# Performance work log

Hardware: AMD Instinct MI355X
Metric: run time of the kernel (lower is better)

Reference implementation:

```python
import jax, jax.numpy as jnp
import numpy as np

DIM = 1024
NUM_HEADS = 8
HEAD_DIM = 64
QK_DIM = NUM_HEADS * HEAD_DIM  # 512
B, S = 4, 1024


def setup_inputs() -> dict:
    key = jax.random.key(0)
    k1, k2, k3, k4, k5 = jax.random.split(key, 5)
    x = jax.random.normal(k1, (B, S, DIM), dtype=jnp.float32)
    mask = jax.random.randint(k2, (B, S), 0, 2).astype(bool)
    rotator = jax.random.normal(k3, (B, S, HEAD_DIM, HEAD_DIM), dtype=jnp.float32)
    # Linear weights stored as [in, out] for x @ W
    w_t = jax.random.normal(k4, (DIM, 2 * QK_DIM + DIM), dtype=jnp.float32) * (DIM ** -0.5)
    w_o = jax.random.normal(k5, (DIM, DIM), dtype=jnp.float32) * (DIM ** -0.5)
    return {"x": x, "mask": mask, "rotator": rotator, "w_t": w_t, "w_o": w_o}


def taylor_atn_fn(qs, ks, vs, mask):
    # 2nd-order Taylor approximation of softmax attention:
    # exp(s) ~= 1 + s + s^2/2, with invalid keys masked out.
    scale = HEAD_DIM ** -0.5
    s = jnp.einsum('bqhd,bkhd->bhqk', qs, ks) * scale  # [B,H,S,S]
    scores = 1.0 + s + 0.5 * s * s
    scores = scores * mask[:, None, None, :].astype(scores.dtype)  # mask keys
    denom = jnp.maximum(jnp.sum(scores, axis=-1), 1e-6)            # [B,H,Q]
    out = jnp.einsum('bhqk,bkhd->bqhd', scores, vs)
    out = out / jnp.transpose(denom, (0, 2, 1))[..., None]         # [B,Q,H,vd]
    return out.reshape(out.shape[0], out.shape[1], -1)


def reference(x, mask, rotator, w_t, w_o):
    t = x @ w_t                                   # [B,S,2*QK+DIM]
    Bx, Sx = t.shape[0], t.shape[1]
    qs = t[..., :QK_DIM].reshape(Bx, Sx, NUM_HEADS, HEAD_DIM)
    ks = t[..., QK_DIM:2 * QK_DIM].reshape(Bx, Sx, NUM_HEADS, HEAD_DIM)
    vs = t[..., 2 * QK_DIM:].reshape(Bx, Sx, NUM_HEADS, -1)
    m = mask[..., None, None]
    # masked per-position rotation: q -> R q, k -> R^T k
    qs = jnp.where(m, jnp.einsum('bsij,bshj->bshi', rotator, qs), qs)
    ks = jnp.where(m, jnp.einsum('bsij,bshi->bshj', rotator, ks), ks)
    out = taylor_atn_fn(qs, ks, vs, mask)
    return out @ w_o
```

## Files before the change

kernel.cpp:

```cpp
#include <hip/hip_runtime.h>
#include <cstdint>
#include <cstddef>

#define DIMX  1024
#define NH    8
#define HD    64
#define QKD   512
#define VDD   128
#define BATCH 4
#define SEQ   1024
#define NPOS  (BATCH*SEQ)
#define TW    (2*QKD + DIMX)
#define SCALE 0.125f

typedef __bf16 bf16x8 __attribute__((ext_vector_type(8)));
typedef float  f32x4  __attribute__((ext_vector_type(4)));
typedef float  f32x16 __attribute__((ext_vector_type(16)));

__device__ __forceinline__ ushort f2bf(float f) {
    unsigned b = __float_as_uint(f);
    return (ushort)((b + 0x7FFFu + ((b >> 16) & 1u)) >> 16);
}
__device__ __forceinline__ float bf2f(ushort u) {
    return __uint_as_float((unsigned)u << 16);
}

__device__ __forceinline__ unsigned cvtpk(float lo, float hi) {
    unsigned r;
    asm("v_cvt_pk_bf16_f32 %0, %1, %2" : "=v"(r) : "v"(lo), "v"(hi));
    return r;
}

__device__ __forceinline__ void plswap(unsigned &a, unsigned &b) {
    asm("v_permlane32_swap_b32 %0, %1" : "+v"(a), "+v"(b));
}

#define GLD16(src, dst) __builtin_amdgcn_global_load_lds(                      \
    (const __attribute__((address_space(1))) unsigned int*)(src),              \
    (__attribute__((address_space(3))) unsigned int*)(dst), 16, 0, 0)

#define SW(row, col) ((row)*64 + ((col) ^ (((row)&7)<<3)))

__device__ __forceinline__ int2 xcd_swz(int gx, int gy) {
    const int nwg = gx * gy;
    int id = blockIdx.y * gx + blockIdx.x;
    id = (id & 7) * (nwg >> 3) + (id >> 3);
    return make_int2(id % gx, id / gx);
}

__global__ __launch_bounds__(256)
void prep_all(const float* __restrict__ x, const float* __restrict__ w_t,
              const float* __restrict__ w_o, ushort* __restrict__ xbf,
              ushort* __restrict__ wtT, ushort* __restrict__ woT)
{
    __shared__ float tile[32][33];
    const int bid = blockIdx.x;
    if (bid < 2048) {
        const size_t i = ((size_t)bid * 256 + threadIdx.x) * 8;
        float4 v0 = *(const float4*)(x + i);
        float4 v1 = *(const float4*)(x + i + 4);
        ushort o[8] = {f2bf(v0.x), f2bf(v0.y), f2bf(v0.z), f2bf(v0.w),
                       f2bf(v1.x), f2bf(v1.y), f2bf(v1.z), f2bf(v1.w)};
        *(uint4*)(xbf + i) = *(uint4*)o;
        return;
    }
    const float* W; ushort* WT; int K, N, bn, bk;
    if (bid < 4096) {
        W = w_t; WT = wtT; K = DIMX; N = TW;
        const int t = bid - 2048;
        bn = (t & 63) * 32; bk = (t >> 6) * 32;
    } else {
        W = w_o; WT = woT; K = DIMX; N = DIMX;
        const int t = bid - 4096;
        bn = (t & 31) * 32; bk = (t >> 5) * 32;
    }
    const int tx = threadIdx.x & 31;
    const int ty = threadIdx.x >> 5;
    #pragma unroll
    for (int i = ty; i < 32; i += 8)
        tile[i][tx] = W[(size_t)(bk + i) * N + bn + tx];
    __syncthreads();
    #pragma unroll
    for (int i = ty; i < 32; i += 8)
        WT[(size_t)(bn + i) * K + bk + tx] = f2bf(tile[tx][i]);
}

#define GEMM_PROLOGUE(Aptr, Bptr, Kdim)                                        \
    __shared__ __align__(16) ushort lA[2 * 128 * 64];                          \
    __shared__ __align__(16) ushort lB[2 * 128 * 64];                          \
    const int tid  = threadIdx.x;                                              \
    const int lane = tid & 63;                                                 \
    const int wave = tid >> 6;                                                 \
    const int wr   = wave >> 1;                                                \
    const int wc   = wave & 1;                                                 \
    const int rsub = lane >> 3;                        \
    const int scol = ((lane & 7) * 8) ^ ((rsub & 7) << 3);                     \
    const ushort* aP = (Aptr) + (size_t)(bm + wave*32 + rsub) * (Kdim) + scol; \
    const ushort* bP = (Bptr) + (size_t)(bn + wave*32 + rsub) * (Kdim) + scol; \
    ushort* lAw = lA + wave * 2048;                                            \
    ushort* lBw = lB + wave * 2048;                                            \
    const int fr = lane & 15;                                                  \
    const int l4 = lane >> 4;                                                  \
    f32x4 acc[4][4] = {};

#define GSTAGE(buf, k0, Kdim)                                                  \
    do {                                                                       \
        _Pragma("unroll")                                                      \
        for (int c = 0; c < 4; ++c) {                                          \
            GLD16(aP + (size_t)(c*8) * (Kdim) + (k0), lAw + (buf)*8192 + c*512);\
            GLD16(bP + (size_t)(c*8) * (Kdim) + (k0), lBw + (buf)*8192 + c*512);\
        }                                                                      \
    } while (0)

#define GEMM_KLOOP(Kdim)                                                       \
    GSTAGE(0, 0, Kdim);                                                        \
    for (int t = 0; t < (Kdim)/64; ++t) {                                      \
        const int cur = t & 1;                                                 \
        if (t < (Kdim)/64 - 1) {                                               \
            GSTAGE(cur ^ 1, (t + 1) * 64, Kdim);                               \
            asm volatile("s_waitcnt vmcnt(8)" ::: "memory");                   \
        } else {                                                               \
            asm volatile("s_waitcnt vmcnt(0)" ::: "memory");                   \
        }                                                                      \
        __builtin_amdgcn_s_barrier();               \
        _Pragma("unroll")                                                      \
        for (int ks = 0; ks < 2; ++ks) {                                       \
            bf16x8 af[4], bfr[4];                                              \
            _Pragma("unroll")                                                  \
            for (int m = 0; m < 4; ++m)                                        \
                af[m] = *(const bf16x8*)&lA[cur*8192 +                         \
                    SW(wr*64 + m*16 + fr, ks*32 + l4*8)];                      \
            _Pragma("unroll")                                                  \
            for (int n = 0; n < 4; ++n)                                        \
                bfr[n] = *(const bf16x8*)&lB[cur*8192 +                        \
                    SW(wc*64 + n*16 + fr, ks*32 + l4*8)];                      \
            _Pragma("unroll")                                                  \
            for (int m = 0; m < 4; ++m)                                        \
                _Pragma("unroll")                                              \
                for (int n = 0; n < 4; ++n)                                    \
                    acc[m][n] = __builtin_amdgcn_mfma_f32_16x16x32_bf16(       \
                        af[m], bfr[n], acc[m][n], 0, 0, 0);                    \
        }                                                                      \
        asm volatile("s_waitcnt lgkmcnt(0)" ::: "memory");                     \
        __builtin_amdgcn_s_barrier();             \
    }

__global__ __launch_bounds__(256, 2)
void gemm_qkv(const ushort* __restrict__ A, const ushort* __restrict__ BT,
              ushort* __restrict__ t1b, ushort* __restrict__ Vt)
{
    const int2 bij = xcd_swz(TW/128, NPOS/128);
    const int bm = bij.y * 128;
    const int bn = bij.x * 128;
    GEMM_PROLOGUE(A, BT, DIMX)
    GEMM_KLOOP(DIMX)

    const int orow = l4 * 4;
    if (bn < 1024) {
        #pragma unroll
        for (int m = 0; m < 4; ++m)
            #pragma unroll
            for (int n = 0; n < 4; ++n) {
                ushort* dst = t1b + (size_t)(bm + wr * 64 + m * 16 + orow) * 1024
                                  + bn + wc * 64 + n * 16 + fr;
                #pragma unroll
                for (int q = 0; q < 4; ++q)
                    dst[(size_t)q * 1024] = f2bf(acc[m][n][q]);
            }
    } else {
        #pragma unroll
        for (int m = 0; m < 4; ++m)
            #pragma unroll
            for (int n = 0; n < 4; ++n) {
                const int row0 = bm + wr * 64 + m * 16 + orow;
                const int cv   = bn + wc * 64 + n * 16 + fr - 1024;
                const int hh = cv >> 7, vd = cv & 127;
                const int bb = row0 >> 10, ss = row0 & 1023;
                ushort o4[4];
                #pragma unroll
                for (int q = 0; q < 4; ++q) o4[q] = f2bf(acc[m][n][q]);
                *(ushort4*)&Vt[((size_t)(bb*NH + hh)*VDD + vd)*SEQ + ss] =
                    *(ushort4*)o4;
            }
    }
}

__global__ __launch_bounds__(256, 2)
void gemm_bf16_mfma(const ushort* __restrict__ A, const ushort* __restrict__ BT,
                    float* __restrict__ C)
{
    const int2 bij = xcd_swz(DIMX/128, NPOS/128);
    const int bm = bij.y * 128;
    const int bn = bij.x * 128;
    GEMM_PROLOGUE(A, BT, DIMX)
    GEMM_KLOOP(DIMX)

    const int orow = l4 * 4;
    #pragma unroll
    for (int m = 0; m < 4; ++m)
        #pragma unroll
        for (int n = 0; n < 4; ++n) {
            float* dst = C + (size_t)(bm + wr * 64 + m * 16 + orow) * DIMX
                           + bn + wc * 64 + n * 16 + fr;
            #pragma unroll
            for (int q = 0; q < 4; ++q)
                dst[(size_t)q * DIMX] = acc[m][n][q];
        }
}

__global__ __launch_bounds__(256)
void rotate_pack_qk(const ushort* __restrict__ t1b, const int* __restrict__ mask,
                    const float* __restrict__ rot, ushort* __restrict__ Qb,
                    ushort* __restrict__ Kb)
{
    const int p   = blockIdx.x;
    const int tid = threadIdx.x;
    const int b = p >> 10, s = p & 1023;
    const bool rotated = (mask[p] != 0);

    __shared__ float R[64][69];
    __shared__ float qv[QKD];
    __shared__ float kv[QKD];

    const ushort* tq = t1b + (size_t)p * 1024;
    {
        ushort2 q2 = *(const ushort2*)(tq + tid*2);
        ushort2 k2 = *(const ushort2*)(tq + QKD + tid*2);
        qv[tid*2]   = bf2f(q2.x); qv[tid*2+1] = bf2f(q2.y);
        kv[tid*2]   = bf2f(k2.x); kv[tid*2+1] = bf2f(k2.y);
        if (rotated) {
            const float* Rg = rot + (size_t)p * 4096;
            const int base = tid * 16;
            const int r = base >> 6, c = base & 63;
            #pragma unroll
            for (int x = 0; x < 16; x += 4) {
                float4 v = *(const float4*)(Rg + base + x);
                R[r][c+x+0] = v.x; R[r][c+x+1] = v.y;
                R[r][c+x+2] = v.z; R[r][c+x+3] = v.w;
            }
        }
    }
    __syncthreads();

    #pragma unroll
    for (int ph = 0; ph < 2; ++ph) {
        const int h = (tid >> 6) + ph*4;
        const int i = tid & 63;
        const float* qh  = &qv[h*64];
        const float* kh2 = &kv[h*64];
        float aq, ak;
        if (rotated) {
            aq = 0.f; ak = 0.f;
            #pragma unroll 8
            for (int j = 0; j < 64; ++j) {
                aq = fmaf(R[i][j], qh[j], aq);
                ak = fmaf(R[j][i], kh2[j], ak);
            }
        } else {
            aq = qh[i]; ak = kh2[i];
        }
        const size_t dst = ((size_t)(b*NH + h)*SEQ + s)*HD + i;
        Qb[dst] = f2bf(aq * SCALE);
        Kb[dst] = f2bf(ak);
    }
}

__global__ __launch_bounds__(256, 2)
void taylor_attn_mfma(const ushort* __restrict__ Qb, const ushort* __restrict__ Kb,
                      const ushort* __restrict__ Vt, const int* __restrict__ mask,
                      ushort* __restrict__ attn)
{
    const int bh  = blockIdx.x;
    const int qt  = blockIdx.y;
    const int b   = bh >> 3, h = bh & 7;
    const int tid = threadIdx.x;
    const int lane = tid & 63;
    const int wave = tid >> 6;
    const int kh  = wave >> 1;
    const int qg  = wave & 1;
    const int l31 = lane & 31;
    const int g   = lane >> 5;

    __shared__ __align__(16) ushort smem[32768];
    __shared__ float mskAll[SEQ];
    __shared__ float dpart[64];
    __shared__ float dinv2[64];

    ushort* Ksp = smem + kh * 8192;
    ushort* Vsp = smem + 16384 + kh * 8192;
    float*  comb = (float*)smem;

    {
        int4 mv = *(const int4*)(mask + b*SEQ + tid*4);
        float4 f = make_float4(mv.x ? 1.f : 0.f, mv.y ? 1.f : 0.f,
                               mv.z ? 1.f : 0.f, mv.w ? 1.f : 0.f);
        *(float4*)&mskAll[tid*4] = f;
    }

    const ushort* qrow = Qb + ((size_t)bh*SEQ + qt*64 + qg*32 + l31) * HD + g*8;
    bf16x8 qf[4];
    #pragma unroll
    for (int ds = 0; ds < 4; ++ds) qf[ds] = *(const bf16x8*)(qrow + ds*16);

    const int sub  = lane >> 3;
    const int scol = ((lane & 7) * 8) ^ (sub << 3);
    const ushort* Kbase = Kb + (size_t)bh*SEQ*HD;
    const ushort* Vbase = Vt + (size_t)bh*VDD*SEQ;

#define ISSUE_K(buf, ktn) do {                                                 \
    _Pragma("unroll")                                                          \
    for (int i_ = 0; i_ < 4; ++i_)                                             \
        GLD16(Kbase + ((size_t)(ktn)*64 + 8*(qg*4+i_) + sub)*HD + scol,        \
              Ksp + (buf)*4096 + (qg*4+i_)*512);                               \
} while (0)
#define ISSUE_V(ktn) do {                                                      \
    _Pragma("unroll")                                                          \
    for (int i_ = 0; i_ < 8; ++i_)                                             \
        GLD16(Vbase + (size_t)(8*(qg*8+i_) + sub)*SEQ + (ktn)*64 + scol,       \
              Vsp + (qg*8+i_)*512);                                            \
} while (0)

    f32x16 acc[4] = {};
    float dacc = 0.f;

    __syncthreads();
    ISSUE_K(0, kh*8);

    for (int it = 0; it < 8; ++it) {
        const int kt = kh*8 + it;
        const int cb = it & 1;
        ISSUE_V(kt);
        if (it < 7) {
            ISSUE_K(cb ^ 1, kt + 1);
            asm volatile("s_waitcnt vmcnt(12)" ::: "memory");
        } else {
            asm volatile("s_waitcnt vmcnt(8)"  ::: "memory");
        }
        __builtin_amdgcn_s_barrier();

        f32x16 sf0 = {}, sf1 = {};
        __builtin_amdgcn_s_setprio(1);
        #pragma unroll
        for (int ds = 0; ds < 4; ++ds) {
            const int dc = ds*16 + g*8;
            bf16x8 kf0 = *(const bf16x8*)&Ksp[cb*4096 + SW(l31, dc)];
            bf16x8 kf1 = *(const bf16x8*)&Ksp[cb*4096 + SW(32 + l31, dc)];
            sf0 = __builtin_amdgcn_mfma_f32_32x32x16_bf16(kf0, qf[ds], sf0, 0, 0, 0);
            sf1 = __builtin_amdgcn_mfma_f32_32x32x16_bf16(kf1, qf[ds], sf1, 0, 0, 0);
        }
        __builtin_amdgcn_s_setprio(0);

        const float* mrow = mskAll + kt*64;
        unsigned w0[8], w1[8];
        float dadd = 0.f;
        #pragma unroll
        for (int rr = 0; rr < 4; ++rr) {
            const float4 mqa = *(const float4*)&mrow[8*rr + 4*g];
            const float4 mqb = *(const float4*)&mrow[32 + 8*rr + 4*g];
            float s0 = sf0[rr*4+0], s1 = sf0[rr*4+1];
            float s2 = sf0[rr*4+2], s3 = sf0[rr*4+3];
            float c0 = fmaf(fmaf(0.5f*s0, s0, s0), mqa.x, mqa.x);
            float c1 = fmaf(fmaf(0.5f*s1, s1, s1), mqa.y, mqa.y);
            float c2 = fmaf(fmaf(0.5f*s2, s2, s2), mqa.z, mqa.z);
            float c3 = fmaf(fmaf(0.5f*s3, s3, s3), mqa.w, mqa.w);
            float t0 = sf1[rr*4+0], t1 = sf1[rr*4+1];
            float t2 = sf1[rr*4+2], t3 = sf1[rr*4+3];
            float d0 = fmaf(fmaf(0.5f*t0, t0, t0), mqb.x, mqb.x);
            float d1 = fmaf(fmaf(0.5f*t1, t1, t1), mqb.y, mqb.y);
            float d2 = fmaf(fmaf(0.5f*t2, t2, t2), mqb.z, mqb.z);
            float d3 = fmaf(fmaf(0.5f*t3, t3, t3), mqb.w, mqb.w);
            dadd += ((c0+c1)+(c2+c3)) + ((d0+d1)+(d2+d3));
            w0[rr*2+0] = cvtpk(c0, c1);
            w0[rr*2+1] = cvtpk(c2, c3);
            w1[rr*2+0] = cvtpk(d0, d1);
            w1[rr*2+1] = cvtpk(d2, d3);
        }
        dacc += dadd;
        plswap(w0[0], w0[2]); plswap(w0[1], w0[3]);
        plswap(w0[4], w0[6]); plswap(w0[5], w0[7]);
        plswap(w1[0], w1[2]); plswap(w1[1], w1[3]);
        plswap(w1[4], w1[6]); plswap(w1[5], w1[7]);

        if (it < 7) asm volatile("s_waitcnt vmcnt(4)" ::: "memory");
        else        asm volatile("s_waitcnt vmcnt(0)" ::: "memory");
        __builtin_amdgcn_s_barrier();

        __builtin_amdgcn_s_setprio(1);
        #pragma unroll
        for (int kq = 0; kq < 4; ++kq) {
            union { unsigned u[4]; bf16x8 v; } pu;
            if (kq == 0)      { pu.u[0]=w0[0]; pu.u[1]=w0[1]; pu.u[2]=w0[2]; pu.u[3]=w0[3]; }
            else if (kq == 1) { pu.u[0]=w0[4]; pu.u[1]=w0[5]; pu.u[2]=w0[6]; pu.u[3]=w0[7]; }
            else if (kq == 2) { pu.u[0]=w1[0]; pu.u[1]=w1[1]; pu.u[2]=w1[2]; pu.u[3]=w1[3]; }
            else              { pu.u[0]=w1[4]; pu.u[1]=w1[5]; pu.u[2]=w1[6]; pu.u[3]=w1[7]; }
            const int kcol = kq*16 + g*8;
            acc[0] = __builtin_amdgcn_mfma_f32_32x32x16_bf16(
                pu.v, *(const bf16x8*)&Vsp[SW(      l31, kcol)], acc[0], 0, 0, 0);
            acc[1] = __builtin_amdgcn_mfma_f32_32x32x16_bf16(
                pu.v, *(const bf16x8*)&Vsp[SW( 32 + l31, kcol)], acc[1], 0, 0, 0);
            acc[2] = __builtin_amdgcn_mfma_f32_32x32x16_bf16(
                pu.v, *(const bf16x8*)&Vsp[SW( 64 + l31, kcol)], acc[2], 0, 0, 0);
            acc[3] = __builtin_amdgcn_mfma_f32_32x32x16_bf16(
                pu.v, *(const bf16x8*)&Vsp[SW( 96 + l31, kcol)], acc[3], 0, 0, 0);
        }
        __builtin_amdgcn_s_setprio(0);
        __builtin_amdgcn_s_barrier();
    }
#undef ISSUE_K
#undef ISSUE_V

    const float dhalf = dacc + __shfl_xor(dacc, 32);

    if (kh == 1) {
        float* cbp = comb + qg * 4096;
        #pragma unroll
        for (int vb = 0; vb < 4; ++vb)
            #pragma unroll
            for (int rr = 0; rr < 4; ++rr) {
                float4 v = make_float4(acc[vb][rr*4+0], acc[vb][rr*4+1],
                                       acc[vb][rr*4+2], acc[vb][rr*4+3]);
                *(float4*)&cbp[(vb*32 + l31)*32 + 4*g + 8*rr] = v;
            }
        if (lane < 32) dpart[qg*32 + l31] = dhalf;
    }
    __syncthreads();
    if (kh == 0) {
        float* cbp = comb + qg * 4096;
        const float dtot = dhalf + dpart[qg*32 + l31];
        if (lane < 32) dinv2[qg*32 + l31] = 1.f / fmaxf(dtot, 1e-6f);
        #pragma unroll
        for (int vb = 0; vb < 4; ++vb)
            #pragma unroll
            for (int rr = 0; rr < 4; ++rr) {
                float4 v = *(const float4*)&cbp[(vb*32 + l31)*32 + 4*g + 8*rr];
                acc[vb][rr*4+0] += v.x; acc[vb][rr*4+1] += v.y;
                acc[vb][rr*4+2] += v.z; acc[vb][rr*4+3] += v.w;
            }
        float inv[16];
        #pragma unroll
        for (int rr = 0; rr < 4; ++rr) {
            float4 iv = *(const float4*)&dinv2[qg*32 + 8*rr + 4*g];
            inv[rr*4+0] = iv.x; inv[rr*4+1] = iv.y;
            inv[rr*4+2] = iv.z; inv[rr*4+3] = iv.w;
        }
        ushort* obase = attn + ((size_t)(b*SEQ + qt*64 + qg*32)) * DIMX
                      + h*VDD + l31;
        #pragma unroll
        for (int vb = 0; vb < 4; ++vb)
            #pragma unroll
            for (int rr = 0; rr < 4; ++rr)
                #pragma unroll
                for (int j = 0; j < 4; ++j) {
                    const int q = 4*g + 8*rr + j;
                    obase[(size_t)q*DIMX + vb*32] = f2bf(acc[vb][rr*4+j] * inv[rr*4+j]);
                }
    }
}

extern "C" void kernel_launch(void* const* d_in, const int* in_sizes, int n_in,
                              void* d_out, int out_size, void* d_ws, size_t ws_size,
                              hipStream_t stream)
{
    const float* x    = (const float*)d_in[0];
    const int*   mask = (const int*)d_in[1];
    const float* rot  = (const float*)d_in[2];
    const float* w_t  = (const float*)d_in[3];
    const float* w_o  = (const float*)d_in[4];
    float* out = (float*)d_out;

    ushort* t1b    = (ushort*)d_ws;
    ushort* xbf    = t1b + (size_t)NPOS * 1024;
    ushort* attnbf = xbf;
    ushort* wtT    = xbf + (size_t)NPOS * DIMX;
    ushort* woT    = wtT + (size_t)TW * DIMX;
    ushort* Qb     = woT + (size_t)DIMX * DIMX;
    ushort* Kb     = Qb  + (size_t)BATCH * NH * SEQ * HD;
    ushort* Vtp    = Kb  + (size_t)BATCH * NH * SEQ * HD;

    prep_all<<<5120, 256, 0, stream>>>(x, w_t, w_o, xbf, wtT, woT);

    gemm_qkv<<<dim3(TW/128, NPOS/128), 256, 0, stream>>>(xbf, wtT, t1b, Vtp);
    rotate_pack_qk<<<NPOS, 256, 0, stream>>>(t1b, mask, rot, Qb, Kb);
    taylor_attn_mfma<<<dim3(BATCH*NH, SEQ/64), 256, 0, stream>>>(Qb, Kb, Vtp, mask, attnbf);
    gemm_bf16_mfma<<<dim3(DIMX/128, NPOS/128), 256, 0, stream>>>(attnbf, woT, out);
}
```

Baseline: 97.38 us.

## Compact valid keys and values so attention skips masked key tiles

Adds a per-batch prefix scan of the key mask to compute compacted positions and a valid-key count. The QKV GEMM epilogue and the rotate kernel scatter only valid K and V rows into compacted buffers, and the attention kernel loops over only ceil(nvalid/64) key tiles, masking by index against nvalid. This is meant to roughly halve attention work for a random mask, at the cost of scattered 2-byte V stores, an extra scan, and reading compacted tail rows past nvalid that are never written.

```diff
diff --git a/kernel.cpp b/kernel.cpp
--- a/kernel.cpp
+++ b/kernel.cpp
@@ -50,11 +50,39 @@
 
 __global__ __launch_bounds__(256)
 void prep_all(const float* __restrict__ x, const float* __restrict__ w_t,
-              const float* __restrict__ w_o, ushort* __restrict__ xbf,
-              ushort* __restrict__ wtT, ushort* __restrict__ woT)
+              const float* __restrict__ w_o, const int* __restrict__ mask,
+              ushort* __restrict__ xbf, ushort* __restrict__ wtT,
+              ushort* __restrict__ woT, int* __restrict__ cpos,
+              int* __restrict__ nvalid)
 {
     __shared__ float tile[32][33];
     const int bid = blockIdx.x;
+    if (bid >= 5120) {
+        const int b = bid - 5120;
+        int* part = (int*)tile;
+        const int t = threadIdx.x;
+        int4 m = *(const int4*)(mask + b*SEQ + t*4);
+        const int v0 = (m.x != 0), v1 = (m.y != 0);
+        const int v2 = (m.z != 0), v3 = (m.w != 0);
+        const int mine = v0 + v1 + v2 + v3;
+        part[t] = mine;
+        __syncthreads();
+        for (int off = 1; off < 256; off <<= 1) {
+            int y = (t >= off) ? part[t - off] : 0;
+            __syncthreads();
+            part[t] += y;
+            __syncthreads();
+        }
+        const int ex = part[t] - mine;
+        int4 o;
+        o.x = v0 ? ex : -1;
+        o.y = v1 ? ex + v0 : -1;
+        o.z = v2 ? ex + v0 + v1 : -1;
+        o.w = v3 ? ex + v0 + v1 + v2 : -1;
+        *(int4*)(cpos + b*SEQ + t*4) = o;
+        if (t == 255) nvalid[b] = part[255];
+        return;
+    }
     if (bid < 2048) {
         const size_t i = ((size_t)bid * 256 + threadIdx.x) * 8;
         float4 v0 = *(const float4*)(x + i);
@@ -147,7 +175,8 @@
 
 __global__ __launch_bounds__(256, 2)
 void gemm_qkv(const ushort* __restrict__ A, const ushort* __restrict__ BT,
-              ushort* __restrict__ t1b, ushort* __restrict__ Vt)
+              ushort* __restrict__ t1b, ushort* __restrict__ Vc,
+              const int* __restrict__ cpos)
 {
     const int2 bij = xcd_swz(TW/128, NPOS/128);
     const int bm = bij.y * 128;
@@ -176,11 +205,12 @@
                 const int cv   = bn + wc * 64 + n * 16 + fr - 1024;
                 const int hh = cv >> 7, vd = cv & 127;
                 const int bb = row0 >> 10, ss = row0 & 1023;
-                ushort o4[4];
-                #pragma unroll
-                for (int q = 0; q < 4; ++q) o4[q] = f2bf(acc[m][n][q]);
-                *(ushort4*)&Vt[((size_t)(bb*NH + hh)*VDD + vd)*SEQ + ss] =
-                    *(ushort4*)o4;
+                int4 cp = *(const int4*)(cpos + bb*SEQ + ss);
+                ushort* vrow = Vc + ((size_t)(bb*NH + hh)*VDD + vd)*SEQ;
+                if (cp.x >= 0) vrow[cp.x] = f2bf(acc[m][n][0]);
+                if (cp.y >= 0) vrow[cp.y] = f2bf(acc[m][n][1]);
+                if (cp.z >= 0) vrow[cp.z] = f2bf(acc[m][n][2]);
+                if (cp.w >= 0) vrow[cp.w] = f2bf(acc[m][n][3]);
             }
     }
 }
@@ -211,12 +241,13 @@
 __global__ __launch_bounds__(256)
 void rotate_pack_qk(const ushort* __restrict__ t1b, const int* __restrict__ mask,
                     const float* __restrict__ rot, ushort* __restrict__ Qb,
-                    ushort* __restrict__ Kb)
+                    ushort* __restrict__ Kc, const int* __restrict__ cpos)
 {
     const int p   = blockIdx.x;
     const int tid = threadIdx.x;
     const int b = p >> 10, s = p & 1023;
     const bool rotated = (mask[p] != 0);
+    const int cp = cpos[p];
 
     __shared__ float R[64][69];
     __shared__ float qv[QKD];
@@ -259,15 +290,15 @@
         } else {
             aq = qh[i]; ak = kh2[i];
         }
-        const size_t dst = ((size_t)(b*NH + h)*SEQ + s)*HD + i;
-        Qb[dst] = f2bf(aq * SCALE);
-        Kb[dst] = f2bf(ak);
+        Qb[((size_t)(b*NH + h)*SEQ + s)*HD + i] = f2bf(aq * SCALE);
+        if (rotated)
+            Kc[((size_t)(b*NH + h)*SEQ + cp)*HD + i] = f2bf(ak);
     }
 }
 
 __global__ __launch_bounds__(256, 2)
-void taylor_attn_mfma(const ushort* __restrict__ Qb, const ushort* __restrict__ Kb,
-                      const ushort* __restrict__ Vt, const int* __restrict__ mask,
+void taylor_attn_mfma(const ushort* __restrict__ Qb, const ushort* __restrict__ Kc,
+                      const ushort* __restrict__ Vc, const int* __restrict__ nvalid,
                       ushort* __restrict__ attn)
 {
     const int bh  = blockIdx.x;
@@ -282,7 +313,6 @@
     const int g   = lane >> 5;
 
     __shared__ __align__(16) ushort smem[32768];
-    __shared__ float mskAll[SEQ];
     __shared__ float dpart[64];
     __shared__ float dinv2[64];
 
@@ -290,12 +320,9 @@
     ushort* Vsp = smem + 16384 + kh * 8192;
     float*  comb = (float*)smem;
 
-    {
-        int4 mv = *(const int4*)(mask + b*SEQ + tid*4);
-        float4 f = make_float4(mv.x ? 1.f : 0.f, mv.y ? 1.f : 0.f,
-                               mv.z ? 1.f : 0.f, mv.w ? 1.f : 0.f);
-        *(float4*)&mskAll[tid*4] = f;
-    }
+    const int nv = nvalid[b];
+    const int T  = (nv + 63) >> 6;
+    const int Th = (T + 1) >> 1;
 
     const ushort* qrow = Qb + ((size_t)bh*SEQ + qt*64 + qg*32 + l31) * HD + g*8;
     bf16x8 qf[4];
@@ -304,8 +331,8 @@
 
     const int sub  = lane >> 3;
     const int scol = ((lane & 7) * 8) ^ (sub << 3);
-    const ushort* Kbase = Kb + (size_t)bh*SEQ*HD;
-    const ushort* Vbase = Vt + (size_t)bh*VDD*SEQ;
+    const ushort* Kbase = Kc + (size_t)bh*SEQ*HD;
+    const ushort* Vbase = Vc + (size_t)bh*VDD*SEQ;
 
 #define ISSUE_K(buf, ktn) do {                                                 \
     _Pragma("unroll")                                                          \
@@ -323,14 +350,14 @@
     f32x16 acc[4] = {};
     float dacc = 0.f;
 
-    __syncthreads();
-    ISSUE_K(0, kh*8);
-
-    for (int it = 0; it < 8; ++it) {
-        const int kt = kh*8 + it;
+    asm volatile("s_waitcnt vmcnt(0)" ::: "memory");
+    ISSUE_K(0, kh*Th);
+
+    for (int it = 0; it < Th; ++it) {
+        const int kt = kh*Th + it;
         const int cb = it & 1;
         ISSUE_V(kt);
-        if (it < 7) {
+        if (it < Th - 1) {
             ISSUE_K(cb ^ 1, kt + 1);
             asm volatile("s_waitcnt vmcnt(12)" ::: "memory");
         } else {
@@ -350,25 +377,32 @@
         }
         __builtin_amdgcn_s_setprio(0);
 
-        const float* mrow = mskAll + kt*64;
+        const int kb0 = kt*64 + 4*g;
         unsigned w0[8], w1[8];
         float dadd = 0.f;
         #pragma unroll
         for (int rr = 0; rr < 4; ++rr) {
-            const float4 mqa = *(const float4*)&mrow[8*rr + 4*g];
-            const float4 mqb = *(const float4*)&mrow[32 + 8*rr + 4*g];
+            const int ka = kb0 + 8*rr;
+            const float ma0 = (ka + 0 < nv) ? 1.f : 0.f;
+            const float ma1 = (ka + 1 < nv) ? 1.f : 0.f;
+            const float ma2 = (ka + 2 < nv) ? 1.f : 0.f;
+            const float ma3 = (ka + 3 < nv) ? 1.f : 0.f;
+            const float mb0 = (ka + 32 < nv) ? 1.f : 0.f;
+            const float mb1 = (ka + 33 < nv) ? 1.f : 0.f;
+            const float mb2 = (ka + 34 < nv) ? 1.f : 0.f;
+            const float mb3 = (ka + 35 < nv) ? 1.f : 0.f;
             float s0 = sf0[rr*4+0], s1 = sf0[rr*4+1];
             float s2 = sf0[rr*4+2], s3 = sf0[rr*4+3];
-            float c0 = fmaf(fmaf(0.5f*s0, s0, s0), mqa.x, mqa.x);
-            float c1 = fmaf(fmaf(0.5f*s1, s1, s1), mqa.y, mqa.y);
-            float c2 = fmaf(fmaf(0.5f*s2, s2, s2), mqa.z, mqa.z);
-            float c3 = fmaf(fmaf(0.5f*s3, s3, s3), mqa.w, mqa.w);
+            float c0 = fmaf(fmaf(0.5f*s0, s0, s0), ma0, ma0);
+            float c1 = fmaf(fmaf(0.5f*s1, s1, s1), ma1, ma1);
+            float c2 = fmaf(fmaf(0.5f*s2, s2, s2), ma2, ma2);
+            float c3 = fmaf(fmaf(0.5f*s3, s3, s3), ma3, ma3);
             float t0 = sf1[rr*4+0], t1 = sf1[rr*4+1];
             float t2 = sf1[rr*4+2], t3 = sf1[rr*4+3];
-            float d0 = fmaf(fmaf(0.5f*t0, t0, t0), mqb.x, mqb.x);
-            float d1 = fmaf(fmaf(0.5f*t1, t1, t1), mqb.y, mqb.y);
-            float d2 = fmaf(fmaf(0.5f*t2, t2, t2), mqb.z, mqb.z);
-            float d3 = fmaf(fmaf(0.5f*t3, t3, t3), mqb.w, mqb.w);
+            float d0 = fmaf(fmaf(0.5f*t0, t0, t0), mb0, mb0);
+            float d1 = fmaf(fmaf(0.5f*t1, t1, t1), mb1, mb1);
+            float d2 = fmaf(fmaf(0.5f*t2, t2, t2), mb2, mb2);
+            float d3 = fmaf(fmaf(0.5f*t3, t3, t3), mb3, mb3);
             dadd += ((c0+c1)+(c2+c3)) + ((d0+d1)+(d2+d3));
             w0[rr*2+0] = cvtpk(c0, c1);
             w0[rr*2+1] = cvtpk(c2, c3);
@@ -381,8 +415,8 @@
         plswap(w1[0], w1[2]); plswap(w1[1], w1[3]);
         plswap(w1[4], w1[6]); plswap(w1[5], w1[7]);
 
-        if (it < 7) asm volatile("s_waitcnt vmcnt(4)" ::: "memory");
-        else        asm volatile("s_waitcnt vmcnt(0)" ::: "memory");
+        if (it < Th - 1) asm volatile("s_waitcnt vmcnt(4)" ::: "memory");
+        else             asm volatile("s_waitcnt vmcnt(0)" ::: "memory");
         __builtin_amdgcn_s_barrier();
 
         __builtin_amdgcn_s_setprio(1);
@@ -474,13 +508,17 @@
     ushort* wtT    = xbf + (size_t)NPOS * DIMX;
     ushort* woT    = wtT + (size_t)TW * DIMX;
     ushort* Qb     = woT + (size_t)DIMX * DIMX;
-    ushort* Kb     = Qb  + (size_t)BATCH * NH * SEQ * HD;
-    ushort* Vtp    = Kb  + (size_t)BATCH * NH * SEQ * HD;
-
-    prep_all<<<5120, 256, 0, stream>>>(x, w_t, w_o, xbf, wtT, woT);
-
-    gemm_qkv<<<dim3(TW/128, NPOS/128), 256, 0, stream>>>(xbf, wtT, t1b, Vtp);
-    rotate_pack_qk<<<NPOS, 256, 0, stream>>>(t1b, mask, rot, Qb, Kb);
-    taylor_attn_mfma<<<dim3(BATCH*NH, SEQ/64), 256, 0, stream>>>(Qb, Kb, Vtp, mask, attnbf);
+    ushort* Kc     = Qb  + (size_t)BATCH * NH * SEQ * HD;
+    ushort* Vc     = Kc  + (size_t)BATCH * NH * SEQ * HD;
+    int*    cpos   = (int*)(Vc + (size_t)BATCH * NH * VDD * SEQ);
+    int*    nvalid = cpos + NPOS;
+
+    prep_all<<<5124, 256, 0, stream>>>(x, w_t, w_o, mask, xbf, wtT, woT,
+                                       cpos, nvalid);
+
+    gemm_qkv<<<dim3(TW/128, NPOS/128), 256, 0, stream>>>(xbf, wtT, t1b, Vc, cpos);
+    rotate_pack_qk<<<NPOS, 256, 0, stream>>>(t1b, mask, rot, Qb, Kc, cpos);
+    taylor_attn_mfma<<<dim3(BATCH*NH, SEQ/64), 256, 0, stream>>>(Qb, Kc, Vc,
+                                                                 nvalid, attnbf);
     gemm_bf16_mfma<<<dim3(DIMX/128, NPOS/128), 256, 0, stream>>>(attnbf, woT, out);
 }
```

Result: no change. 97.44 us (+0.1%).
